# Performance work log

Hardware: AMD Instinct MI355X
Metric: run time of the kernel (lower is better)

## Reference

```python
import jax, jax.numpy as jnp
import numpy as np

N, K, D, DOUT = 100000, 16, 128, 128

def setup_inputs() -> dict:
    key = jax.random.key(0)
    k1, k2, k3 = jax.random.split(key, 3)
    self_vecs = jax.random.normal(k1, (N, D), dtype=jnp.float32)
    neigh_vecs = jax.random.normal(k2, (N, K, D), dtype=jnp.float32)
    # glorot([input_dim, output_dim])
    limit = np.sqrt(6.0 / (D + DOUT)).astype(np.float32)
    weights = jax.random.uniform(k3, (D, DOUT), dtype=jnp.float32, minval=-limit, maxval=limit)
    return {"self_vecs": self_vecs, "neigh_vecs": neigh_vecs, "weights": weights}

def reference(self_vecs, neigh_vecs, weights):
    # concat self node as an extra "neighbor": [N, K+1, D]
    neigh_self = jnp.concatenate([neigh_vecs, self_vecs[:, None, :]], axis=1)
    # attention scores: query is the self vector, keys are neighbors+self -> [N, K+1]
    score = jnp.einsum('nd,nkd->nk', self_vecs, neigh_self)
    attn = jax.nn.softmax(score, axis=-1)
    # weighted sum of values -> [N, D]
    context = jnp.einsum('nk,nkd->nd', attn, neigh_self)
    out = context @ weights  # [N, DOUT]
    return jax.nn.relu(out)
```

## Files before the change

kernel.cpp:

```cpp
#include <hip/hip_runtime.h>


constexpr int K    = 16;
constexpr int D    = 128;
constexpr int DOUT = 128;
constexpr int WT_PITCH = 136;

typedef short bfrag  __attribute__((ext_vector_type(8)));
typedef float afrag  __attribute__((ext_vector_type(4)));

__device__ __forceinline__ unsigned short f2bf(float f) {
    union { float f; unsigned u; } v; v.f = f;
    const unsigned r = v.u + 0x7FFF + ((v.u >> 16) & 1);
    return (unsigned short)(r >> 16);
}
__device__ __forceinline__ float bf2f(unsigned short b) {
    union { unsigned u; float f; } v; v.u = ((unsigned)b) << 16;
    return v.f;
}

__device__ __forceinline__ float half_allsum(float x) {
    #pragma unroll
    for (int off = 1; off <= 16; off <<= 1)
        x += __shfl_xor(x, off);
    return x;
}

__launch_bounds__(512, 2)
__global__ void gat_fused(const float* __restrict__ self_vecs,
                          const float* __restrict__ neigh_vecs,
                          const float* __restrict__ W,
                          float* __restrict__ out,
                          int n_tiles) {
    __shared__ __align__(16) unsigned short Wt[DOUT][WT_PITCH];
    __shared__ __align__(16) unsigned short Chl[2][2][16][WT_PITCH];

    const int tid = threadIdx.x;

    for (int e = tid; e < D * DOUT; e += blockDim.x) {
        const int k = e >> 7, m = e & 127;
        Wt[m][k] = f2bf(W[e]);
    }
    __syncthreads();

    const int lane = tid & 63;
    const int wid  = tid >> 6;
    const int half = lane >> 5;
    const int q    = lane & 31;
    const int nl   = lane & 15;
    const int kb   = lane >> 4;
    const int r0   = wid * 2;

    float4 v[K], sv;

    int buf = 0;
    int t = blockIdx.x;

    if (t < n_tiles) {
        const int n0 = t * 16 + r0 + half;
        const float4* nb = (const float4*)(neigh_vecs + (size_t)n0 * (K * D)) + q;
        #pragma unroll
        for (int k = 0; k < K; ++k) v[k] = nb[k * 32];
        sv = ((const float4*)(self_vecs + (size_t)n0 * D))[q];
    }

    for (; t < n_tiles; t += gridDim.x, buf ^= 1) {
        const int node0 = t * 16;
        const int tn  = t + gridDim.x;
        const int tl  = (tn < n_tiles) ? tn : t;
        const int nn0 = tl * 16 + r0 + half;
        const float4* nbN = (const float4*)(neigh_vecs + (size_t)nn0 * (K * D)) + q;

        float ss = half_allsum(sv.x * sv.x + sv.y * sv.y + sv.z * sv.z + sv.w * sv.w);
        float sum = 1.f;
        float4 cx = sv;
        #pragma unroll
        for (int k = 0; k < K; ++k) {
            float p = sv.x * v[k].x + sv.y * v[k].y + sv.z * v[k].z + sv.w * v[k].w;
            p = half_allsum(p);
            const float e = __expf(p - ss);
            sum += e;
            cx.x += e * v[k].x; cx.y += e * v[k].y;
            cx.z += e * v[k].z; cx.w += e * v[k].w;
            v[k] = nbN[k * 32];
        }
        sv = ((const float4*)(self_vecs + (size_t)nn0 * D))[q];

        const float inv = 1.f / sum;
        const float cf[4] = {cx.x * inv, cx.y * inv, cx.z * inv, cx.w * inv};

        unsigned short hi4[4], lo4[4];
        #pragma unroll
        for (int i = 0; i < 4; ++i) {
            hi4[i] = f2bf(cf[i]);
            lo4[i] = f2bf(cf[i] - bf2f(hi4[i]));
        }
        *(uint2*)&Chl[buf][0][r0 + half][4 * q] = *(const uint2*)hi4;
        *(uint2*)&Chl[buf][1][r0 + half][4 * q] = *(const uint2*)lo4;

        __syncthreads();

        afrag acc;
        #pragma unroll
        for (int r4 = 0; r4 < 4; ++r4) acc[r4] = 0.f;

        #pragma unroll
        for (int kc = 0; kc < 4; ++kc) {
            const bfrag ch = *(const bfrag*)&Chl[buf][0][nl][kc * 32 + kb * 8];
            const bfrag cl = *(const bfrag*)&Chl[buf][1][nl][kc * 32 + kb * 8];
            const bfrag a  = *(const bfrag*)&Wt[wid * 16 + nl][kc * 32 + kb * 8];
            acc = __builtin_amdgcn_mfma_f32_16x16x32_bf16(a, ch, acc, 0, 0, 0);
            acc = __builtin_amdgcn_mfma_f32_16x16x32_bf16(a, cl, acc, 0, 0, 0);
        }
        float* orow = out + (size_t)(node0 + nl) * DOUT + kb * 4;
        *(float4*)(orow + wid * 16) =
            make_float4(fmaxf(acc[0], 0.f), fmaxf(acc[1], 0.f),
                        fmaxf(acc[2], 0.f), fmaxf(acc[3], 0.f));
    }
}

extern "C" void kernel_launch(void* const* d_in, const int* in_sizes, int n_in,
                              void* d_out, int out_size, void* d_ws, size_t ws_size,
                              hipStream_t stream) {
    const float* self_vecs = (const float*)d_in[0];
    const float* neigh     = (const float*)d_in[1];
    const float* W         = (const float*)d_in[2];
    float* out = (float*)d_out;

    const int n_nodes = in_sizes[0] / D;
    const int n_tiles = n_nodes / 16;

    const int tpb = 512;
    const int blocks = 512;
    gat_fused<<<dim3(blocks), dim3(tpb), 0, stream>>>(
        self_vecs, neigh, W, out, n_tiles);
}
```

Measured before the change: 190.0 us.

## Keep W fragments in registers and process two node tiles per barrier

Removes the shared-memory copy of the transposed bf16 weights. Each wave now loads its W fragments once into registers, which cuts LDS traffic and LDS footprint. The loop handles 32 nodes (two 16-node tiles) per iteration, so there is one __syncthreads per two tiles instead of one per tile. The risks are higher register pressure (a[4] plus the v[16] prefetch) and an uncoalesced strided global read of W at startup. Because n_stiles = N/32 = 3125 evenly, the tail behaviour is unchanged.

```diff
diff --git a/kernel.cpp b/kernel.cpp
--- a/kernel.cpp
+++ b/kernel.cpp
@@ -4,7 +4,7 @@
 constexpr int K    = 16;
 constexpr int D    = 128;
 constexpr int DOUT = 128;
-constexpr int WT_PITCH = 136;
+constexpr int CT_PITCH = 136;
 
 typedef short bfrag  __attribute__((ext_vector_type(8)));
 typedef float afrag  __attribute__((ext_vector_type(4)));
@@ -31,18 +31,10 @@
                           const float* __restrict__ neigh_vecs,
                           const float* __restrict__ W,
                           float* __restrict__ out,
-                          int n_tiles) {
-    __shared__ __align__(16) unsigned short Wt[DOUT][WT_PITCH];
-    __shared__ __align__(16) unsigned short Chl[2][2][16][WT_PITCH];
+                          int n_stiles) {
+    __shared__ __align__(16) unsigned short Chl[2][2][2][16][CT_PITCH];
 
-    const int tid = threadIdx.x;
-
-    for (int e = tid; e < D * DOUT; e += blockDim.x) {
-        const int k = e >> 7, m = e & 127;
-        Wt[m][k] = f2bf(W[e]);
-    }
-    __syncthreads();
-
+    const int tid  = threadIdx.x;
     const int lane = tid & 63;
     const int wid  = tid >> 6;
     const int half = lane >> 5;
@@ -51,71 +43,88 @@
     const int kb   = lane >> 4;
     const int r0   = wid * 2;
 
+    bfrag a[4];
+    #pragma unroll
+    for (int kc = 0; kc < 4; ++kc)
+        #pragma unroll
+        for (int i = 0; i < 8; ++i) {
+            const int k = kc * 32 + kb * 8 + i;
+            a[kc][i] = (short)f2bf(W[k * DOUT + wid * 16 + nl]);
+        }
+
     float4 v[K], sv;
 
     int buf = 0;
-    int t = blockIdx.x;
+    int st = blockIdx.x;
 
-    if (t < n_tiles) {
-        const int n0 = t * 16 + r0 + half;
+    if (st < n_stiles) {
+        const int n0 = st * 32 + r0 + half;
         const float4* nb = (const float4*)(neigh_vecs + (size_t)n0 * (K * D)) + q;
         #pragma unroll
         for (int k = 0; k < K; ++k) v[k] = nb[k * 32];
         sv = ((const float4*)(self_vecs + (size_t)n0 * D))[q];
     }
 
-    for (; t < n_tiles; t += gridDim.x, buf ^= 1) {
-        const int node0 = t * 16;
-        const int tn  = t + gridDim.x;
-        const int tl  = (tn < n_tiles) ? tn : t;
-        const int nn0 = tl * 16 + r0 + half;
-        const float4* nbN = (const float4*)(neigh_vecs + (size_t)nn0 * (K * D)) + q;
+    for (; st < n_stiles; st += gridDim.x, buf ^= 1) {
+        #pragma unroll
+        for (int tt = 0; tt < 2; ++tt) {
+            int rs, rt;
+            if (tt == 0) { rs = st; rt = 1; }
+            else {
+                const int sn = st + gridDim.x;
+                rs = (sn < n_stiles) ? sn : st;
+                rt = 0;
+            }
+            const int rn = (rs * 2 + rt) * 16 + r0 + half;
+            const float4* nbN = (const float4*)(neigh_vecs + (size_t)rn * (K * D)) + q;
 
-        float ss = half_allsum(sv.x * sv.x + sv.y * sv.y + sv.z * sv.z + sv.w * sv.w);
-        float sum = 1.f;
-        float4 cx = sv;
-        #pragma unroll
-        for (int k = 0; k < K; ++k) {
-            float p = sv.x * v[k].x + sv.y * v[k].y + sv.z * v[k].z + sv.w * v[k].w;
-            p = half_allsum(p);
-            const float e = __expf(p - ss);
-            sum += e;
-            cx.x += e * v[k].x; cx.y += e * v[k].y;
-            cx.z += e * v[k].z; cx.w += e * v[k].w;
-            v[k] = nbN[k * 32];
+            float ss = half_allsum(sv.x * sv.x + sv.y * sv.y + sv.z * sv.z + sv.w * sv.w);
+            float sum = 1.f;
+            float4 cx = sv;
+            #pragma unroll
+            for (int k = 0; k < K; ++k) {
+                float p = sv.x * v[k].x + sv.y * v[k].y + sv.z * v[k].z + sv.w * v[k].w;
+                p = half_allsum(p);
+                const float e = __expf(p - ss);
+                sum += e;
+                cx.x += e * v[k].x; cx.y += e * v[k].y;
+                cx.z += e * v[k].z; cx.w += e * v[k].w;
+                v[k] = nbN[k * 32];
+            }
+            sv = ((const float4*)(self_vecs + (size_t)rn * D))[q];
+
+            const float inv = 1.f / sum;
+            const float cf[4] = {cx.x * inv, cx.y * inv, cx.z * inv, cx.w * inv};
+            unsigned short hi4[4], lo4[4];
+            #pragma unroll
+            for (int i = 0; i < 4; ++i) {
+                hi4[i] = f2bf(cf[i]);
+                lo4[i] = f2bf(cf[i] - bf2f(hi4[i]));
+            }
+            *(uint2*)&Chl[buf][tt][0][r0 + half][4 * q] = *(const uint2*)hi4;
+            *(uint2*)&Chl[buf][tt][1][r0 + half][4 * q] = *(const uint2*)lo4;
         }
-        sv = ((const float4*)(self_vecs + (size_t)nn0 * D))[q];
-
-        const float inv = 1.f / sum;
-        const float cf[4] = {cx.x * inv, cx.y * inv, cx.z * inv, cx.w * inv};
-
-        unsigned short hi4[4], lo4[4];
-        #pragma unroll
-        for (int i = 0; i < 4; ++i) {
-            hi4[i] = f2bf(cf[i]);
-            lo4[i] = f2bf(cf[i] - bf2f(hi4[i]));
-        }
-        *(uint2*)&Chl[buf][0][r0 + half][4 * q] = *(const uint2*)hi4;
-        *(uint2*)&Chl[buf][1][r0 + half][4 * q] = *(const uint2*)lo4;
 
         __syncthreads();
 
-        afrag acc;
         #pragma unroll
-        for (int r4 = 0; r4 < 4; ++r4) acc[r4] = 0.f;
-
-        #pragma unroll
-        for (int kc = 0; kc < 4; ++kc) {
-            const bfrag ch = *(const bfrag*)&Chl[buf][0][nl][kc * 32 + kb * 8];
-            const bfrag cl = *(const bfrag*)&Chl[buf][1][nl][kc * 32 + kb * 8];
-            const bfrag a  = *(const bfrag*)&Wt[wid * 16 + nl][kc * 32 + kb * 8];
-            acc = __builtin_amdgcn_mfma_f32_16x16x32_bf16(a, ch, acc, 0, 0, 0);
-            acc = __builtin_amdgcn_mfma_f32_16x16x32_bf16(a, cl, acc, 0, 0, 0);
+        for (int tt = 0; tt < 2; ++tt) {
+            afrag acc;
+            #pragma unroll
+            for (int r4 = 0; r4 < 4; ++r4) acc[r4] = 0.f;
+            #pragma unroll
+            for (int kc = 0; kc < 4; ++kc) {
+                const bfrag ch = *(const bfrag*)&Chl[buf][tt][0][nl][kc * 32 + kb * 8];
+                const bfrag cl = *(const bfrag*)&Chl[buf][tt][1][nl][kc * 32 + kb * 8];
+                acc = __builtin_amdgcn_mfma_f32_16x16x32_bf16(a[kc], ch, acc, 0, 0, 0);
+                acc = __builtin_amdgcn_mfma_f32_16x16x32_bf16(a[kc], cl, acc, 0, 0, 0);
+            }
+            const int node0t = (st * 2 + tt) * 16;
+            float* orow = out + (size_t)(node0t + nl) * DOUT + kb * 4;
+            *(float4*)(orow + wid * 16) =
+                make_float4(fmaxf(acc[0], 0.f), fmaxf(acc[1], 0.f),
+                            fmaxf(acc[2], 0.f), fmaxf(acc[3], 0.f));
         }
-        float* orow = out + (size_t)(node0 + nl) * DOUT + kb * 4;
-        *(float4*)(orow + wid * 16) =
-            make_float4(fmaxf(acc[0], 0.f), fmaxf(acc[1], 0.f),
-                        fmaxf(acc[2], 0.f), fmaxf(acc[3], 0.f));
     }
 }
 
@@ -127,11 +136,11 @@
     const float* W         = (const float*)d_in[2];
     float* out = (float*)d_out;
 
-    const int n_nodes = in_sizes[0] / D;
-    const int n_tiles = n_nodes / 16;
+    const int n_nodes  = in_sizes[0] / D;
+    const int n_stiles = n_nodes / 32;
 
     const int tpb = 512;
     const int blocks = 512;
     gat_fused<<<dim3(blocks), dim3(tpb), 0, stream>>>(
-        self_vecs, neigh, W, out, n_tiles);
+        self_vecs, neigh, W, out, n_stiles);
 }
```

After: 178.9 us. 5.8% less time.
